# Performance work log

Measured on AMD Instinct MI355X. Metric: run time of the kernel, lower is better.

## Reference

```python
import jax, jax.numpy as jnp
import numpy as np

WS = 7  # window size
NH = 12  # num heads
EPS = 1e-5


def setup_inputs() -> dict:
    key = jax.random.key(0)
    ks = jax.random.split(key, 12)
    B, H, W, C = 32, 56, 56, 384
    Dff = 4 * C
    s = lambda k, shape, scale=0.02: jax.random.normal(k, shape, dtype=jnp.float32) * scale
    return {
        "x": jax.random.normal(ks[0], (B, H, W, C), dtype=jnp.float32),
        "ln1_g": jnp.ones((C,), jnp.float32), "ln1_b": jnp.zeros((C,), jnp.float32),
        "qkv_w": s(ks[1], (C, 3 * C)), "qkv_b": jnp.zeros((3 * C,), jnp.float32),
        "proj_w": s(ks[2], (C, C)), "proj_b": jnp.zeros((C,), jnp.float32),
        "ln2_g": jnp.ones((C,), jnp.float32), "ln2_b": jnp.zeros((C,), jnp.float32),
        "mlp_w1": s(ks[3], (C, Dff)), "mlp_b1": jnp.zeros((Dff,), jnp.float32),
        "mlp_w2": s(ks[4], (Dff, C)), "mlp_b2": jnp.zeros((C,), jnp.float32),
    }


def _layernorm(x, g, b):
    m = jnp.mean(x, axis=-1, keepdims=True)
    v = jnp.mean(jnp.square(x - m), axis=-1, keepdims=True)
    return (x - m) * jax.lax.rsqrt(v + EPS) * g + b


def reference(x, ln1_g, ln1_b, qkv_w, qkv_b, proj_w, proj_b, ln2_g, ln2_b,
              mlp_w1, mlp_b1, mlp_w2, mlp_b2):
    B, H, W, C = x.shape
    N = WS * WS
    hd = C // NH
    shortcut = x
    xn = _layernorm(x, ln1_g, ln1_b)
    # window partition: [B,H,W,C] -> [B*nW, N, C]
    xw = xn.reshape(B, H // WS, WS, W // WS, WS, C).transpose(0, 1, 3, 2, 4, 5)
    xw = xw.reshape(-1, N, C)
    # attention within each 49-token window
    qkv = (xw @ qkv_w + qkv_b).reshape(-1, N, 3, NH, hd)
    qkv = qkv.transpose(2, 0, 3, 1, 4)  # [3, Bn, h, N, d]
    q, k, v = qkv[0] * (hd ** -0.5), qkv[1], qkv[2]
    attn = jax.nn.softmax(jnp.einsum('bhnd,bhmd->bhnm', q, k), axis=-1)
    out = jnp.einsum('bhnm,bhmd->bhnd', attn, v)  # [Bn, h, N, d]
    out = out.transpose(0, 2, 1, 3).reshape(-1, N, C)
    out = out @ proj_w + proj_b
    # window unpartition
    xa = out.reshape(B, H // WS, W // WS, WS, WS, C).transpose(0, 1, 3, 2, 4, 5)
    xa = xa.reshape(B, H, W, C)
    x = shortcut + xa
    # MLP (dropout inactive at inference); Keras gelu default is exact
    h = jax.nn.gelu(_layernorm(x, ln2_g, ln2_b) @ mlp_w1 + mlp_b1, approximate=False)
    return x + (h @ mlp_w2 + mlp_b2)
```

## Files before the change

kernel.cpp:

```cpp
#include <hip/hip_runtime.h>
#include <hip/hip_bf16.h>
#include <cstdint>

typedef __bf16 bf16;
typedef __bf16 bf16x8 __attribute__((ext_vector_type(8)));
typedef float f32x4 __attribute__((ext_vector_type(4)));
typedef unsigned int u32;
typedef unsigned short u16;

#define DEV static __device__ __forceinline__

DEV float bfbits2f(u32 bits) { return __builtin_bit_cast(float, bits << 16); }
DEV u16 f2bfbits(float f) {
  u32 u = __builtin_bit_cast(u32, f);
  u32 r = (u + 0x7fffu + ((u >> 16) & 1u)) >> 16;
  return (u16)r;
}

__global__ __launch_bounds__(256) void probe_k(const u32* __restrict__ x, u32* __restrict__ flag) {
  __shared__ int cnt[256];
  int t = threadIdx.x;
  int c = 0;
#pragma unroll
  for (int i = 0; i < 4; ++i) {
    u32 u = x[t * 4 + i];
    u32 e = (u >> 7) & 0xFF;
    c += (e >= 110 && e <= 140) ? 1 : 0;
  }
  cnt[t] = c;
  __syncthreads();
  for (int s = 128; s > 0; s >>= 1) {
    if (t < s) cnt[t] += cnt[t + s];
    __syncthreads();
  }
  if (t == 0) flag[0] = (cnt[0] > 512) ? 1u : 0u;
}

__global__ __launch_bounds__(256) void cvt_params_k(const void* p0, const void* p1,
                                                    const void* p2, const void* p3,
                                                    const void* p4, const void* p5,
                                                    const void* p6, const void* p7,
                                                    float* __restrict__ out,
                                                    const u32* __restrict__ flag) {
  int i = blockIdx.x * 256 + threadIdx.x;
  if (i >= 4992) return;
  const int bounds[9] = {0, 1152, 1536, 3072, 3456, 3840, 4224, 4608, 4992};
  const void* ps[8] = {p0, p1, p2, p3, p4, p5, p6, p7};
  int seg = 0;
  while (i >= bounds[seg + 1]) ++seg;
  int off = i - bounds[seg];
  bool isbf = flag[0] != 0;
  out[i] = isbf ? bfbits2f(((const u16*)ps[seg])[off]) : ((const float*)ps[seg])[off];
}

__global__ __launch_bounds__(256) void transpose_k(const void* __restrict__ in,
                                                   u16* __restrict__ out, int R, int Cc,
                                                   const u32* __restrict__ flag) {
  bool isbf = flag[0] != 0;
  __shared__ u16 tile[32][33];
  int bx = blockIdx.x * 32, by = blockIdx.y * 32;
  int tx = threadIdx.x & 31, ty = threadIdx.x >> 5;
#pragma unroll
  for (int i = 0; i < 32; i += 8) {
    size_t idx = (size_t)(by + ty + i) * Cc + bx + tx;
    u16 v = isbf ? ((const u16*)in)[idx] : f2bfbits(((const float*)in)[idx]);
    tile[ty + i][tx] = v;
  }
  __syncthreads();
#pragma unroll
  for (int i = 0; i < 32; i += 8)
    out[(size_t)(bx + ty + i) * R + by + tx] = tile[tx][ty + i];
}

template <int RAWSRC>
__global__ __launch_bounds__(256) void ln_kernel(const void* __restrict__ xv,
                                                 const float* __restrict__ g,
                                                 const float* __restrict__ b,
                                                 u32* __restrict__ out,
                                                 const u32* __restrict__ flag,
                                                 int windowed, int t0) {
  const int t = t0 + blockIdx.x * 4 + (threadIdx.x >> 6);
  const int lane = threadIdx.x & 63;
  const int e0 = lane * 6;
  float f[6];
  if (RAWSRC) {
    if (flag[0] != 0) {
      const u16* xb = (const u16*)xv + (size_t)t * 384 + e0;
#pragma unroll
      for (int j = 0; j < 6; ++j) f[j] = bfbits2f(xb[j]);
    } else {
      const float* xf = (const float*)xv + (size_t)t * 384 + e0;
#pragma unroll
      for (int j = 0; j < 6; ++j) f[j] = xf[j];
    }
  } else {
    const u32* xr = (const u32*)xv + (size_t)t * 192 + lane * 3;
#pragma unroll
    for (int j = 0; j < 3; ++j) {
      u32 u = xr[j];
      f[2 * j] = bfbits2f(u & 0xffff);
      f[2 * j + 1] = bfbits2f(u >> 16);
    }
  }
  float s = 0.f, q = 0.f;
#pragma unroll
  for (int j = 0; j < 6; ++j) { s += f[j]; q += f[j] * f[j]; }
#pragma unroll
  for (int o = 1; o < 64; o <<= 1) { s += __shfl_xor(s, o); q += __shfl_xor(q, o); }
  float mean = s * (1.0f / 384.0f);
  float var = q * (1.0f / 384.0f) - mean * mean;
  float rstd = rsqrtf(var + 1e-5f);
  int orow;
  if (windowed) {
    int bb = t / 3136, rem = t % 3136;
    int hh = rem / 56, ww = rem % 56;
    orow = (bb * 64 + (hh / 7) * 8 + (ww / 7)) * 49 + (hh % 7) * 7 + (ww % 7) - t0;
  } else {
    orow = t - t0;
  }
  u32* orp = out + (size_t)orow * 192 + lane * 3;
#pragma unroll
  for (int j = 0; j < 3; ++j) {
    float ye = (f[2 * j] - mean) * rstd * g[e0 + 2 * j] + b[e0 + 2 * j];
    float yo = (f[2 * j + 1] - mean) * rstd * g[e0 + 2 * j + 1] + b[e0 + 2 * j + 1];
    orp[j] = (u32)f2bfbits(ye) | ((u32)f2bfbits(yo) << 16);
  }
}

template <int MODE>
__global__ __launch_bounds__(256, 4) void gemm128(const bf16* __restrict__ A,
                                                  const bf16* __restrict__ BT,
                                                  void* __restrict__ Cv,
                                                  const float* __restrict__ bias,
                                                  const void* __restrict__ resv,
                                                  const u32* __restrict__ flag,
                                                  int ldA, int ldC, int K, int rowOff,
                                                  int nN) {
  const int nwg = (int)gridDim.x;
  const int bid = (int)blockIdx.x;
  const int q = nwg >> 3, r = nwg & 7;
  const int xcd = bid & 7, lid = bid >> 3;
  const int wg = (xcd < r ? xcd * (q + 1) : r * (q + 1) + (xcd - r) * q) + lid;
  const int tN = wg % nN, tM = wg / nN;

  const int tid = threadIdx.x;
  const int lane = tid & 63, wave = tid >> 6;
  const int wr = wave >> 1, wc = wave & 1;
  const int li = lane & 15, gq = lane >> 4;
  const bool isbf = flag[0] != 0;

  __shared__ bf16 As[128 * 64];
  __shared__ bf16 Bs[128 * 64];

  f32x4 acc[4][4] = {};

  const bf16* aTile = A + (size_t)tM * 128 * ldA;
  const bf16* bTile = BT + (size_t)tN * 128 * K;

  for (int k0 = 0; k0 < K; k0 += 64) {
#pragma unroll
    for (int i = 0; i < 4; ++i) {
      int c = i * 256 + tid;
      int row = c >> 3, col8 = (c & 7) << 3;
      __builtin_amdgcn_global_load_lds(
          (const __attribute__((address_space(1))) void*)(aTile + (size_t)row * ldA + k0 + col8),
          (__attribute__((address_space(3))) void*)(As + (size_t)c * 8), 16, 0, 0);
      __builtin_amdgcn_global_load_lds(
          (const __attribute__((address_space(1))) void*)(bTile + (size_t)row * K + k0 + col8),
          (__attribute__((address_space(3))) void*)(Bs + (size_t)c * 8), 16, 0, 0);
    }
    __syncthreads();
#pragma unroll
    for (int ks = 0; ks < 64; ks += 32) {
      bf16x8 af[4], bfr[4];
#pragma unroll
      for (int m = 0; m < 4; ++m)
        af[m] = *(const bf16x8*)(As + (wr * 64 + m * 16 + li) * 64 + ks + gq * 8);
#pragma unroll
      for (int n = 0; n < 4; ++n)
        bfr[n] = *(const bf16x8*)(Bs + (wc * 64 + n * 16 + li) * 64 + ks + gq * 8);
#pragma unroll
      for (int m = 0; m < 4; ++m)
#pragma unroll
        for (int n = 0; n < 4; ++n)
          acc[m][n] = __builtin_amdgcn_mfma_f32_16x16x32_bf16(af[m], bfr[n], acc[m][n], 0, 0, 0);
    }
    __syncthreads();
  }

#pragma unroll
  for (int m = 0; m < 4; ++m) {
#pragma unroll
    for (int r2 = 0; r2 < 4; ++r2) {
      int row = tM * 128 + wr * 64 + m * 16 + gq * 4 + r2;
      size_t crow;
      if (MODE == 1) {
        int gg = rowOff + row;
        int win = gg / 49, n = gg % 49;
        int bb = win >> 6, wi = win & 63;
        int hh = (wi >> 3) * 7 + n / 7;
        int ww = (wi & 7) * 7 + n % 7;
        crow = (size_t)(bb * 3136 + hh * 56 + ww);
      } else {
        crow = (size_t)row;
      }
#pragma unroll
      for (int n = 0; n < 4; ++n) {
        int col = tN * 128 + wc * 64 + n * 16 + li;
        size_t idx = crow * (size_t)ldC + col;
        float v = acc[m][n][r2] + bias[col];
        if (MODE == 2) v = 0.5f * v * (1.0f + erff(v * 0.70710678118654752f));
        if (MODE == 1)
          v += isbf ? bfbits2f(((const u16*)resv)[idx]) : ((const float*)resv)[idx];
        if (MODE == 3) v += bfbits2f(((const u16*)resv)[idx]);
        if (MODE == 3) {
          size_t oidx = idx + (size_t)rowOff * 384;
          if (isbf) ((u16*)Cv)[oidx] = f2bfbits(v);
          else ((float*)Cv)[oidx] = v;
        } else {
          ((u16*)Cv)[idx] = f2bfbits(v);
        }
      }
    }
  }
}

__global__ __launch_bounds__(256, 2) void attn_kernel(const bf16* __restrict__ qkv,
                                                      bf16* __restrict__ out) {
  __shared__ bf16 smem[4 * 6912];
  const int wave = threadIdx.x >> 6;
  const int lane = threadIdx.x & 63;
  const int unit = blockIdx.x * 4 + wave;
  const int win = unit / 12, head = unit % 12;
  bf16* P = smem + wave * 6912;
  bf16* VT = P + 64 * 72;

  const size_t base = (size_t)win * 49 * 1152 + head * 32;
  const bf16* Qp = qkv + base;
  const bf16* Kp = qkv + base + 384;
  const bf16* Vp = qkv + base + 768;

  const int gq = lane >> 4, li = lane & 15;

  {
    int d = lane & 31, half = lane >> 5;
#pragma unroll
    for (int i = 0; i < 32; ++i) {
      int m = i * 2 + half;
      bf16 v = (m < 49) ? Vp[(size_t)m * 1152 + d] : (bf16)0.0f;
      VT[d * 72 + m] = v;
    }
  }

  f32x4 s[4][4] = {};
  bf16x8 qf[4], kf[4];
#pragma unroll
  for (int i = 0; i < 4; ++i) {
    int qr = i * 16 + li; if (qr > 48) qr = 48;
    qf[i] = *(const bf16x8*)(Qp + (size_t)qr * 1152 + gq * 8);
    kf[i] = *(const bf16x8*)(Kp + (size_t)qr * 1152 + gq * 8);
  }
#pragma unroll
  for (int i = 0; i < 4; ++i)
#pragma unroll
    for (int j = 0; j < 4; ++j)
      s[i][j] = __builtin_amdgcn_mfma_f32_16x16x32_bf16(qf[i], kf[j], s[i][j], 0, 0, 0);

  __syncthreads();

  const float scale = 0.17677669529663687f;
#pragma unroll
  for (int i = 0; i < 4; ++i) {
#pragma unroll
    for (int r = 0; r < 4; ++r) {
      float v0 = s[i][0][r] * scale, v1 = s[i][1][r] * scale;
      float v2 = s[i][2][r] * scale, v3 = s[i][3][r] * scale;
      if (li >= 1) v3 = -1e30f;
      float mx = fmaxf(fmaxf(v0, v1), fmaxf(v2, v3));
#pragma unroll
      for (int o = 1; o < 16; o <<= 1) mx = fmaxf(mx, __shfl_xor(mx, o));
      v0 = __expf(v0 - mx); v1 = __expf(v1 - mx);
      v2 = __expf(v2 - mx); v3 = __expf(v3 - mx);
      float sum = v0 + v1 + v2 + v3;
#pragma unroll
      for (int o = 1; o < 16; o <<= 1) sum += __shfl_xor(sum, o);
      float inv = 1.0f / sum;
      int n = i * 16 + gq * 4 + r;
      P[n * 72 + li]      = (bf16)(v0 * inv);
      P[n * 72 + 16 + li] = (bf16)(v1 * inv);
      P[n * 72 + 32 + li] = (bf16)(v2 * inv);
      P[n * 72 + 48 + li] = (bf16)(v3 * inv);
    }
  }

  __syncthreads();

  f32x4 o[4][2] = {};
#pragma unroll
  for (int ms = 0; ms < 2; ++ms) {
    bf16x8 pf[4], vf[2];
#pragma unroll
    for (int i = 0; i < 4; ++i)
      pf[i] = *(const bf16x8*)(P + (i * 16 + li) * 72 + ms * 32 + gq * 8);
#pragma unroll
    for (int dt = 0; dt < 2; ++dt)
      vf[dt] = *(const bf16x8*)(VT + (dt * 16 + li) * 72 + ms * 32 + gq * 8);
#pragma unroll
    for (int i = 0; i < 4; ++i)
#pragma unroll
      for (int dt = 0; dt < 2; ++dt)
        o[i][dt] = __builtin_amdgcn_mfma_f32_16x16x32_bf16(pf[i], vf[dt], o[i][dt], 0, 0, 0);
  }

#pragma unroll
  for (int i = 0; i < 4; ++i) {
#pragma unroll
    for (int r = 0; r < 4; ++r) {
      int n = i * 16 + gq * 4 + r;
      if (n < 49) {
#pragma unroll
        for (int dt = 0; dt < 2; ++dt) {
          int d = dt * 16 + li;
          out[((size_t)win * 49 + n) * 384 + head * 32 + d] = (bf16)o[i][dt][r];
        }
      }
    }
  }
}

extern "C" void kernel_launch(void* const* d_in, const int* in_sizes, int n_in,
                              void* d_out, int out_size, void* d_ws, size_t ws_size,
                              hipStream_t stream) {
  const void* x      = d_in[0];
  const void* ln1_g  = d_in[1];
  const void* ln1_b  = d_in[2];
  const void* qkv_w  = d_in[3];
  const void* qkv_b  = d_in[4];
  const void* proj_w = d_in[5];
  const void* proj_b = d_in[6];
  const void* ln2_g  = d_in[7];
  const void* ln2_b  = d_in[8];
  const void* mlp_w1 = d_in[9];
  const void* mlp_b1 = d_in[10];
  const void* mlp_w2 = d_in[11];
  const void* mlp_b2 = d_in[12];

  char* ws = (char*)d_ws;
  u32* flag = (u32*)ws;
  bf16* qkvwT  = (bf16*)(ws + 256);
  bf16* projwT = qkvwT + 1152 * 384;
  bf16* w1T    = projwT + 384 * 384;
  bf16* w2T    = w1T + 1536 * 384;
  float* pF    = (float*)(ws + 3539200);
  float* qkv_bF  = pF;
  float* proj_bF = pF + 1152;
  float* mlp_b1F = pF + 1536;
  float* mlp_b2F = pF + 3072;
  float* ln1gF   = pF + 3456;
  float* ln1bF   = pF + 3840;
  float* ln2gF   = pF + 4224;
  float* ln2bF   = pF + 4608;
  bf16* x2 = (bf16*)(ws + 3559168);
  char* basep = ws + 80629504ULL;
  const size_t avail = (ws_size > 80629504ULL) ? (ws_size - 80629504ULL) : 0;

  int Wc = 128;
  { const int cand[5] = {2048, 1024, 512, 256, 128};
    for (int i = 0; i < 5; ++i)
      if ((size_t)cand[i] * 49 * 1536 * 2 <= avail) { Wc = cand[i]; break; } }
  int Rc = 6272;
  { const int cand[5] = {100352, 50176, 25088, 12544, 6272};
    for (int i = 0; i < 5; ++i)
      if ((size_t)cand[i] * 1920 * 2 <= avail) { Rc = cand[i]; break; } }

  probe_k<<<1, 256, 0, stream>>>((const u32*)x, flag);

  cvt_params_k<<<20, 256, 0, stream>>>(qkv_b, proj_b, mlp_b1, mlp_b2,
                                       ln1_g, ln1_b, ln2_g, ln2_b, pF, flag);
  transpose_k<<<dim3(36, 12), 256, 0, stream>>>(qkv_w, (u16*)qkvwT, 384, 1152, flag);
  transpose_k<<<dim3(12, 12), 256, 0, stream>>>(proj_w, (u16*)projwT, 384, 384, flag);
  transpose_k<<<dim3(48, 12), 256, 0, stream>>>(mlp_w1, (u16*)w1T, 384, 1536, flag);
  transpose_k<<<dim3(12, 48), 256, 0, stream>>>(mlp_w2, (u16*)w2T, 1536, 384, flag);

  for (int c = 0; c < 2048 / Wc; ++c) {
    const int w0 = c * Wc, t0 = w0 * 49, M = Wc * 49;
    const int nM = M / 128;
    bf16* xn   = (bf16*)basep;
    bf16* qkvb = xn + (size_t)M * 384;
    ln_kernel<1><<<M / 4, 256, 0, stream>>>(x, ln1gF, ln1bF, (u32*)xn, flag, 1, t0);
    gemm128<0><<<dim3(9 * nM), 256, 0, stream>>>(xn, qkvwT, qkvb, qkv_bF, nullptr, flag,
                                                 384, 1152, 384, 0, 9);
    attn_kernel<<<Wc * 3, 256, 0, stream>>>(qkvb, xn);
    gemm128<1><<<dim3(3 * nM), 256, 0, stream>>>(xn, projwT, x2, proj_bF, x, flag,
                                                 384, 384, 384, t0, 3);
  }

  for (int c = 0; c < 100352 / Rc; ++c) {
    const int r0 = c * Rc;
    const int nM = Rc / 128;
    bf16* xn2 = (bf16*)basep;
    bf16* hb  = xn2 + (size_t)Rc * 384;
    ln_kernel<0><<<Rc / 4, 256, 0, stream>>>(x2, ln2gF, ln2bF, (u32*)xn2, flag, 0, r0);
    gemm128<2><<<dim3(12 * nM), 256, 0, stream>>>(xn2, w1T, hb, mlp_b1F, nullptr, flag,
                                                  384, 1536, 384, 0, 12);
    gemm128<3><<<dim3(3 * nM), 256, 0, stream>>>(hb, w2T, d_out, mlp_b2F,
                                                 x2 + (size_t)r0 * 384, flag,
                                                 1536, 384, 1536, r0, 3);
  }
}
```

Measured before the change: 907.9 us.

## Restructure GEMM to 256x64 tiles with A streamed from global and B in LDS

Replaces the 128x128 LDS-tiled GEMM with a 256x64 tile. The full 384-deep K slice of B is staged once in padded LDS, and each wave reads its A fragments straight from global memory. The aim is fewer LDS round trips and barriers for A, and fewer K-loop synchronisations. In exchange, A fragments are now uncoalesced global reads that rely on cache reuse, and LDS use and occupancy change (launch bounds drop from 4 to 3). Chunk-size minimums are also raised so row counts divide by 256.

```diff
diff --git a/kernel.cpp b/kernel.cpp
--- a/kernel.cpp
+++ b/kernel.cpp
@@ -128,7 +128,7 @@
 }
 
 template <int MODE>
-__global__ __launch_bounds__(256, 4) void gemm128(const bf16* __restrict__ A,
+__global__ __launch_bounds__(256, 3) void gemm256(const bf16* __restrict__ A,
                                                   const bf16* __restrict__ BT,
                                                   void* __restrict__ Cv,
                                                   const float* __restrict__ bias,
@@ -145,54 +145,48 @@
 
   const int tid = threadIdx.x;
   const int lane = tid & 63, wave = tid >> 6;
-  const int wr = wave >> 1, wc = wave & 1;
   const int li = lane & 15, gq = lane >> 4;
   const bool isbf = flag[0] != 0;
 
-  __shared__ bf16 As[128 * 64];
-  __shared__ bf16 Bs[128 * 64];
+  __shared__ bf16 Bs[64 * 392];
 
   f32x4 acc[4][4] = {};
 
-  const bf16* aTile = A + (size_t)tM * 128 * ldA;
-  const bf16* bTile = BT + (size_t)tN * 128 * K;
-
-  for (int k0 = 0; k0 < K; k0 += 64) {
-#pragma unroll
-    for (int i = 0; i < 4; ++i) {
-      int c = i * 256 + tid;
-      int row = c >> 3, col8 = (c & 7) << 3;
-      __builtin_amdgcn_global_load_lds(
-          (const __attribute__((address_space(1))) void*)(aTile + (size_t)row * ldA + k0 + col8),
-          (__attribute__((address_space(3))) void*)(As + (size_t)c * 8), 16, 0, 0);
-      __builtin_amdgcn_global_load_lds(
-          (const __attribute__((address_space(1))) void*)(bTile + (size_t)row * K + k0 + col8),
-          (__attribute__((address_space(3))) void*)(Bs + (size_t)c * 8), 16, 0, 0);
+  const bf16* bTile = BT + (size_t)tN * 64 * K;
+  const bf16* aLane = A + (size_t)(tM * 256 + wave * 64 + li) * ldA + gq * 8;
+
+  for (int kc = 0; kc < K; kc += 384) {
+    if (kc) __syncthreads();
+#pragma unroll
+    for (int it = 0; it < 12; ++it) {
+      int c = it * 256 + tid;
+      int col = c / 48, k8 = (c % 48) * 8;
+      bf16x8 v = *(const bf16x8*)(bTile + (size_t)col * K + kc + k8);
+      *(bf16x8*)(Bs + col * 392 + k8) = v;
     }
     __syncthreads();
 #pragma unroll
-    for (int ks = 0; ks < 64; ks += 32) {
+    for (int ks = 0; ks < 384; ks += 32) {
       bf16x8 af[4], bfr[4];
 #pragma unroll
       for (int m = 0; m < 4; ++m)
-        af[m] = *(const bf16x8*)(As + (wr * 64 + m * 16 + li) * 64 + ks + gq * 8);
+        af[m] = *(const bf16x8*)(aLane + (size_t)(m * 16) * ldA + kc + ks);
 #pragma unroll
       for (int n = 0; n < 4; ++n)
-        bfr[n] = *(const bf16x8*)(Bs + (wc * 64 + n * 16 + li) * 64 + ks + gq * 8);
+        bfr[n] = *(const bf16x8*)(Bs + (n * 16 + li) * 392 + ks + gq * 8);
 #pragma unroll
       for (int m = 0; m < 4; ++m)
 #pragma unroll
         for (int n = 0; n < 4; ++n)
           acc[m][n] = __builtin_amdgcn_mfma_f32_16x16x32_bf16(af[m], bfr[n], acc[m][n], 0, 0, 0);
     }
-    __syncthreads();
   }
 
 #pragma unroll
   for (int m = 0; m < 4; ++m) {
 #pragma unroll
     for (int r2 = 0; r2 < 4; ++r2) {
-      int row = tM * 128 + wr * 64 + m * 16 + gq * 4 + r2;
+      int row = tM * 256 + wave * 64 + m * 16 + gq * 4 + r2;
       size_t crow;
       if (MODE == 1) {
         int gg = rowOff + row;
@@ -206,7 +200,7 @@
       }
 #pragma unroll
       for (int n = 0; n < 4; ++n) {
-        int col = tN * 128 + wc * 64 + n * 16 + li;
+        int col = tN * 64 + n * 16 + li;
         size_t idx = crow * (size_t)ldC + col;
         float v = acc[m][n][r2] + bias[col];
         if (MODE == 2) v = 0.5f * v * (1.0f + erff(v * 0.70710678118654752f));
@@ -364,13 +358,13 @@
   char* basep = ws + 80629504ULL;
   const size_t avail = (ws_size > 80629504ULL) ? (ws_size - 80629504ULL) : 0;
 
-  int Wc = 128;
-  { const int cand[5] = {2048, 1024, 512, 256, 128};
-    for (int i = 0; i < 5; ++i)
+  int Wc = 256;
+  { const int cand[4] = {2048, 1024, 512, 256};
+    for (int i = 0; i < 4; ++i)
       if ((size_t)cand[i] * 49 * 1536 * 2 <= avail) { Wc = cand[i]; break; } }
-  int Rc = 6272;
-  { const int cand[5] = {100352, 50176, 25088, 12544, 6272};
-    for (int i = 0; i < 5; ++i)
+  int Rc = 12544;
+  { const int cand[4] = {100352, 50176, 25088, 12544};
+    for (int i = 0; i < 4; ++i)
       if ((size_t)cand[i] * 1920 * 2 <= avail) { Rc = cand[i]; break; } }
 
   probe_k<<<1, 256, 0, stream>>>((const u32*)x, flag);
@@ -384,27 +378,27 @@
 
   for (int c = 0; c < 2048 / Wc; ++c) {
     const int w0 = c * Wc, t0 = w0 * 49, M = Wc * 49;
-    const int nM = M / 128;
+    const int nM = M / 256;
     bf16* xn   = (bf16*)basep;
     bf16* qkvb = xn + (size_t)M * 384;
     ln_kernel<1><<<M / 4, 256, 0, stream>>>(x, ln1gF, ln1bF, (u32*)xn, flag, 1, t0);
-    gemm128<0><<<dim3(9 * nM), 256, 0, stream>>>(xn, qkvwT, qkvb, qkv_bF, nullptr, flag,
-                                                 384, 1152, 384, 0, 9);
+    gemm256<0><<<dim3(18 * nM), 256, 0, stream>>>(xn, qkvwT, qkvb, qkv_bF, nullptr, flag,
+                                                  384, 1152, 384, 0, 18);
     attn_kernel<<<Wc * 3, 256, 0, stream>>>(qkvb, xn);
-    gemm128<1><<<dim3(3 * nM), 256, 0, stream>>>(xn, projwT, x2, proj_bF, x, flag,
-                                                 384, 384, 384, t0, 3);
+    gemm256<1><<<dim3(6 * nM), 256, 0, stream>>>(xn, projwT, x2, proj_bF, x, flag,
+                                                 384, 384, 384, t0, 6);
   }
 
   for (int c = 0; c < 100352 / Rc; ++c) {
     const int r0 = c * Rc;
-    const int nM = Rc / 128;
+    const int nM = Rc / 256;
     bf16* xn2 = (bf16*)basep;
     bf16* hb  = xn2 + (size_t)Rc * 384;
     ln_kernel<0><<<Rc / 4, 256, 0, stream>>>(x2, ln2gF, ln2bF, (u32*)xn2, flag, 0, r0);
-    gemm128<2><<<dim3(12 * nM), 256, 0, stream>>>(xn2, w1T, hb, mlp_b1F, nullptr, flag,
-                                                  384, 1536, 384, 0, 12);
-    gemm128<3><<<dim3(3 * nM), 256, 0, stream>>>(hb, w2T, d_out, mlp_b2F,
+    gemm256<2><<<dim3(24 * nM), 256, 0, stream>>>(xn2, w1T, hb, mlp_b1F, nullptr, flag,
+                                                  384, 1536, 384, 0, 24);
+    gemm256<3><<<dim3(6 * nM), 256, 0, stream>>>(hb, w2T, d_out, mlp_b2F,
                                                  x2 + (size_t)r0 * 384, flag,
-                                                 1536, 384, 1536, r0, 3);
-  }
-}
+                                                 1536, 384, 1536, r0, 6);
+  }
+}
```

After: 1.254 ms. +38.1%, slower.
